# Optimization experiments

Measured on AMD Instinct MI355X. Metric: run time of the kernel, lower is better.

Reference implementation:

```python
import jax, jax.numpy as jnp
import numpy as np

LEAK = 0.95
THRESHOLD = 1.0
CLAMP = 3.0
LN_EPS = 1e-5


def setup_inputs() -> dict:
    key = jax.random.key(0)
    k1, k2 = jax.random.split(key)
    B, S, V, D = 8, 2048, 57344, 1536
    token_ids = jax.random.randint(k1, (B, S), 0, V, dtype=jnp.int64)
    emb_table = jax.random.normal(k2, (V, D), dtype=jnp.float32) * 0.02
    gamma = jnp.ones((D,), dtype=jnp.float32)
    beta = jnp.zeros((D,), dtype=jnp.float32)
    return {"token_ids": token_ids, "emb_table": emb_table, "gamma": gamma, "beta": beta}


def _layernorm(x, gamma, beta):
    mu = jnp.mean(x, axis=-1, keepdims=True)
    var = jnp.mean(jnp.square(x - mu), axis=-1, keepdims=True)
    return (x - mu) * jax.lax.rsqrt(var + LN_EPS) * gamma + beta


def _lif_scan(x):
    # x: [B, S, D]; sequential LIF recurrence over time axis S
    B, S, D = x.shape
    v0 = jnp.zeros((B, D), dtype=x.dtype)

    def step(v, xt):
        v = v * LEAK + xt
        v = jnp.clip(v, -CLAMP, CLAMP)
        spike = (v >= THRESHOLD).astype(x.dtype)
        return v * (1.0 - spike), spike

    _, spikes = jax.lax.scan(step, v0, jnp.swapaxes(x, 0, 1))  # spikes: [S, B, D]
    return jnp.swapaxes(spikes, 0, 1)


def reference(token_ids, emb_table, gamma, beta):
    x = emb_table[token_ids]          # [B, S, D] embedding lookup
    x = _layernorm(x, gamma, beta)    # continuous residual stream
    spikes = _lif_scan(x)             # 0/1 spike tensor [B, S, D]
    return spikes, x
```

## Files before the change

### kernel.cpp

```cpp
#include <hip/hip_runtime.h>


constexpr int Bv = 8, Sv = 2048, Dv = 1536;
constexpr int Cn = 32;
constexpr int Ln = Sv / Cn;
constexpr int Wn = 64;
constexpr int BD = Bv * Dv;
constexpr int TNMAX = Ln + Wn;

constexpr size_t FLAG_OFF  = 0;
constexpr size_t STATS_OFF = 64;
constexpr size_t SPEC0_OFF = STATS_OFF + (size_t)2 * Bv * Sv * 8;
constexpr size_t SPEC1_OFF = SPEC0_OFF + (size_t)Cn * BD * 8;
constexpr size_t WS_NEED   = SPEC1_OFF + (size_t)Cn * BD * 8;

__device__ __forceinline__ double ln_x64(float e, double mu, double rs,
                                         double gd, double bd) {
#pragma clang fp contract(off)
    return (((double)e - mu) * rs) * gd + bd;
}
__device__ __forceinline__ double lif_step(double v, double x, bool& spike) {
#pragma clang fp contract(off)
    double vv = v * 0.95;
    vv = vv + x;
    vv = fmin(fmax(vv, -3.0), 3.0);
    spike = (vv >= 1.0);
    return spike ? 0.0 : vv;
}

extern "C" __global__ __launch_bounds__(256)
void detect_tok64(const int* __restrict__ tok, int* __restrict__ flag)
{
    __shared__ int any_nz;
    if (threadIdx.x == 0) any_nz = 0;
    __syncthreads();
    int nz = 0;
    for (int i = threadIdx.x; i < (Bv * Sv) / 2; i += 256) nz |= tok[2 * i + 1];
    if (nz) atomicOr(&any_nz, 1);
    __syncthreads();
    if (threadIdx.x == 0) flag[0] = (any_nz == 0) ? 1 : 0;
}

extern "C" __global__ __launch_bounds__(128)
void ln_stats_kernel(const int* __restrict__ tok,
                     const float* __restrict__ emb,
                     const float* __restrict__ gamma,
                     const float* __restrict__ beta,
                     float* __restrict__ x_out,
                     double* __restrict__ stats,
                     const int* __restrict__ tok64_flag)
{
#pragma clang fp contract(off)
    __shared__ double p1[2], p2[2];

    const int row = blockIdx.x;
    const int t   = threadIdx.x;
    const int lane = t & 63, wave = t >> 6;

    const int shift = tok64_flag[0];
    const long long tk = (long long)tok[(size_t)row << shift];
    const float* src = emb + tk * (long long)Dv;

    float4 xv[3];
#pragma unroll
    for (int k = 0; k < 3; ++k) xv[k] = reinterpret_cast<const float4*>(src)[t + 128 * k];

    double s = 0.0;
#pragma unroll
    for (int k = 0; k < 3; ++k) {
        s += (double)xv[k].x; s += (double)xv[k].y;
        s += (double)xv[k].z; s += (double)xv[k].w;
    }
#pragma unroll
    for (int off = 1; off < 64; off <<= 1) s += __shfl_xor(s, off);
    if (lane == 0) p1[wave] = s;
    __syncthreads();
    const double mu = (p1[0] + p1[1]) / 1536.0;

    double q = 0.0;
#pragma unroll
    for (int k = 0; k < 3; ++k) {
        double d0 = (double)xv[k].x - mu; q += d0 * d0;
        double d1 = (double)xv[k].y - mu; q += d1 * d1;
        double d2 = (double)xv[k].z - mu; q += d2 * d2;
        double d3 = (double)xv[k].w - mu; q += d3 * d3;
    }
#pragma unroll
    for (int off = 1; off < 64; off <<= 1) q += __shfl_xor(q, off);
    if (lane == 0) p2[wave] = q;
    __syncthreads();
    const double var  = (p2[0] + p2[1]) / 1536.0;
    const double rstd = 1.0 / sqrt(var + 1e-5);

    if (t == 0) { stats[2 * row] = mu; stats[2 * row + 1] = rstd; }

    float* dst = x_out + (long long)row * Dv;
#pragma unroll
    for (int k = 0; k < 3; ++k) {
        const int f4 = t + 128 * k;
        const float4 g4 = reinterpret_cast<const float4*>(gamma)[f4];
        const float4 b4 = reinterpret_cast<const float4*>(beta)[f4];
        float4 o;
        o.x = (float)((((double)xv[k].x - mu) * rstd) * (double)g4.x + (double)b4.x);
        o.y = (float)((((double)xv[k].y - mu) * rstd) * (double)g4.y + (double)b4.y);
        o.z = (float)((((double)xv[k].z - mu) * rstd) * (double)g4.z + (double)b4.z);
        o.w = (float)((((double)xv[k].w - mu) * rstd) * (double)g4.w + (double)b4.w);
        reinterpret_cast<float4*>(dst)[f4] = o;
    }
}

extern "C" __global__ __launch_bounds__(256)
void lif64_spec(const int* __restrict__ tok,
                const float* __restrict__ emb,
                const float* __restrict__ gamma,
                const float* __restrict__ beta,
                const double* __restrict__ stats,
                float* __restrict__ spk,
                double* __restrict__ spec_start,
                double* __restrict__ spec_end,
                const int* __restrict__ tok64_flag)
{
    constexpr int DBLK = Dv / 256;
    __shared__ int     tokl[TNMAX];
    __shared__ double2 statl[TNMAX];

    const int t    = threadIdx.x;
    const int bid  = blockIdx.x;
    const int dblk = bid % DBLK;
    const int c    = (bid / DBLK) % Cn;
    const int b    = bid / (DBLK * Cn);
    const int d    = dblk * 256 + t;

    const int s0 = c * Ln;
    const int sw = (c == 0) ? 0 : s0 - Wn;
    const int TN = s0 + Ln - sw;
    const int warm = s0 - sw;
    const int rowbase = b * Sv;

    if (t < TN) {
        const int row = rowbase + sw + t;
        const int shift = tok64_flag[0];
        tokl[t]  = tok[(size_t)row << shift];
        statl[t] = reinterpret_cast<const double2*>(stats)[row];
    }
    __syncthreads();

    const double gd = (double)gamma[d];
    const double bd = (double)beta[d];
    float* sp = spk + (size_t)b * Sv * Dv + d;

    constexpr int U = 8;
    float ecur[U], enxt[U];
#pragma unroll
    for (int k = 0; k < U; ++k)
        ecur[k] = emb[(long long)tokl[k] * Dv + d];

    double v = 0.0, vstart = 0.0;
    for (int i = 0; i < TN; i += U) {
        if (i + U < TN) {
#pragma unroll
            for (int k = 0; k < U; ++k)
                enxt[k] = emb[(long long)tokl[i + U + k] * Dv + d];
        }
#pragma unroll
        for (int k = 0; k < U; ++k) {
            const int idx = i + k;
            if (idx == warm) vstart = v;
            const double2 st = statl[idx];
            const double x = ln_x64(ecur[k], st.x, st.y, gd, bd);
            bool spike;
            const double vn = lif_step(v, x, spike);
            if (idx >= warm)
                __builtin_nontemporal_store(spike ? 1.0f : 0.0f,
                                            &sp[(size_t)(sw + idx) * Dv]);
            v = vn;
        }
#pragma unroll
        for (int k = 0; k < U; ++k) ecur[k] = enxt[k];
    }

    const size_t chain = (size_t)b * Dv + d;
    spec_start[(size_t)c * BD + chain] = vstart;
    spec_end[(size_t)c * BD + chain]   = v;
}

extern "C" __global__ __launch_bounds__(64)
void lif64_fixup(const int* __restrict__ tok,
                 const float* __restrict__ emb,
                 const float* __restrict__ gamma,
                 const float* __restrict__ beta,
                 const double* __restrict__ stats,
                 const double* __restrict__ spec_start,
                 const double* __restrict__ spec_end,
                 float* __restrict__ spk,
                 const int* __restrict__ tok64_flag)
{
    const int gid = blockIdx.x * 64 + threadIdx.x;
    const int b = gid / Dv;
    const int d = gid - b * Dv;
    const int shift = tok64_flag[0];
    const double gd = (double)gamma[d];
    const double bd = (double)beta[d];
    const int rowbase = b * Sv;
    float* sp = spk + (size_t)b * Sv * Dv + d;

    double v = 0.0;
    for (int c = 0; c < Cn; ++c) {
        const double vs = spec_start[(size_t)c * BD + gid];
        const double ve = spec_end[(size_t)c * BD + gid];
        if (v == vs) { v = ve; continue; }
        constexpr int U = 8;
        const int s0 = c * Ln;
        float  ecur[U], enxt[U];
        double mcur[U], mnxt[U], rcur[U], rnxt[U];
#pragma unroll
        for (int k = 0; k < U; ++k) {
            const int row = rowbase + s0 + k;
            const long long tk = (long long)tok[(size_t)row << shift];
            ecur[k] = emb[tk * (long long)Dv + d];
            mcur[k] = stats[2 * row];
            rcur[k] = stats[2 * row + 1];
        }
        for (int i = 0; i < Ln; i += U) {
            if (i + U < Ln) {
#pragma unroll
                for (int k = 0; k < U; ++k) {
                    const int row = rowbase + s0 + i + U + k;
                    const long long tk = (long long)tok[(size_t)row << shift];
                    enxt[k] = emb[tk * (long long)Dv + d];
                    mnxt[k] = stats[2 * row];
                    rnxt[k] = stats[2 * row + 1];
                }
            }
#pragma unroll
            for (int k = 0; k < U; ++k) {
                const double x = ln_x64(ecur[k], mcur[k], rcur[k], gd, bd);
                bool spike;
                v = lif_step(v, x, spike);
                sp[(size_t)(s0 + i + k) * Dv] = spike ? 1.0f : 0.0f;
            }
#pragma unroll
            for (int k = 0; k < U; ++k) {
                ecur[k] = enxt[k]; mcur[k] = mnxt[k]; rcur[k] = rnxt[k];
            }
        }
    }
}

extern "C" __global__ __launch_bounds__(64)
void lif64_seq(const int* __restrict__ tok,
               const float* __restrict__ emb,
               const float* __restrict__ gamma,
               const float* __restrict__ beta,
               const double* __restrict__ stats,
               float* __restrict__ spk,
               const int* __restrict__ tok64_flag)
{
    const int gid = blockIdx.x * 64 + threadIdx.x;
    const int b = gid / Dv;
    const int d = gid - b * Dv;
    const int shift = tok64_flag[0];
    const int rowbase = b * Sv;
    const double gd = (double)gamma[d];
    const double bd = (double)beta[d];
    float* sp = spk + (size_t)b * Sv * Dv + d;

    constexpr int U = 8;
    float  ecur[U], enxt[U];
    double mcur[U], mnxt[U], rcur[U], rnxt[U];
#pragma unroll
    for (int k = 0; k < U; ++k) {
        const int row = rowbase + k;
        const long long tk = (long long)tok[(size_t)row << shift];
        ecur[k] = emb[tk * (long long)Dv + d];
        mcur[k] = stats[2 * row];
        rcur[k] = stats[2 * row + 1];
    }
    double v = 0.0;
    for (int s = 0; s < Sv; s += U) {
        if (s + U < Sv) {
#pragma unroll
            for (int k = 0; k < U; ++k) {
                const int row = rowbase + s + U + k;
                const long long tk = (long long)tok[(size_t)row << shift];
                enxt[k] = emb[tk * (long long)Dv + d];
                mnxt[k] = stats[2 * row];
                rnxt[k] = stats[2 * row + 1];
            }
        }
#pragma unroll
        for (int k = 0; k < U; ++k) {
            const double x = ln_x64(ecur[k], mcur[k], rcur[k], gd, bd);
            bool spike;
            v = lif_step(v, x, spike);
            __builtin_nontemporal_store(spike ? 1.0f : 0.0f, &sp[(size_t)(s + k) * Dv]);
        }
#pragma unroll
        for (int k = 0; k < U; ++k) { ecur[k] = enxt[k]; mcur[k] = mnxt[k]; rcur[k] = rnxt[k]; }
    }
}

extern "C" void kernel_launch(void* const* d_in, const int* in_sizes, int n_in,
                              void* d_out, int out_size, void* d_ws, size_t ws_size,
                              hipStream_t stream)
{
    const int*   tok   = (const int*)  d_in[0];
    const float* emb   = (const float*)d_in[1];
    const float* gamma = (const float*)d_in[2];
    const float* beta  = (const float*)d_in[3];

    float* out = (float*)d_out;
    float* spk = out;
    float* x   = out + (size_t)Bv * Sv * Dv;

    int*    flg   = (int*)((char*)d_ws + FLAG_OFF);
    double* stats = (double*)((char*)d_ws + STATS_OFF);

    detect_tok64<<<1, 256, 0, stream>>>(tok, flg);
    ln_stats_kernel<<<Bv * Sv, 128, 0, stream>>>(tok, emb, gamma, beta, x, stats, flg);

    if (ws_size >= WS_NEED) {
        double* spec0 = (double*)((char*)d_ws + SPEC0_OFF);
        double* spec1 = (double*)((char*)d_ws + SPEC1_OFF);
        lif64_spec<<<Bv * Cn * (Dv / 256), 256, 0, stream>>>(
            tok, emb, gamma, beta, stats, spk, spec0, spec1, flg);
        lif64_fixup<<<BD / 64, 64, 0, stream>>>(
            tok, emb, gamma, beta, stats, spec0, spec1, spk, flg);
    } else {
        lif64_seq<<<BD / 64, 64, 0, stream>>>(tok, emb, gamma, beta, stats, spk, flg);
    }
}
```

Measured before the change: 118.9 us.

## Pack LIF spikes into 64-bit masks and expand in a separate kernel

The speculative and fixup LIF kernels now record each chunk's spikes as a 64-bit mask in workspace instead of writing float spikes directly. A new spike_expand kernel then writes the full float spike tensor once, using nontemporal stores. This keeps the fixup pass from rewriting spike rows it has to recompute, and takes the large strided store traffic off the sequential scan. In exchange it adds a kernel launch and extra workspace. The token-width detection kernel also moves from 256 to 1024 threads.

```diff
diff --git a/kernel.cpp b/kernel.cpp
--- a/kernel.cpp
+++ b/kernel.cpp
@@ -12,7 +12,8 @@
 constexpr size_t STATS_OFF = 64;
 constexpr size_t SPEC0_OFF = STATS_OFF + (size_t)2 * Bv * Sv * 8;
 constexpr size_t SPEC1_OFF = SPEC0_OFF + (size_t)Cn * BD * 8;
-constexpr size_t WS_NEED   = SPEC1_OFF + (size_t)Cn * BD * 8;
+constexpr size_t BITS_OFF  = SPEC1_OFF + (size_t)Cn * BD * 8;
+constexpr size_t WS_NEED   = BITS_OFF + (size_t)Cn * BD * 8;
 
 __device__ __forceinline__ double ln_x64(float e, double mu, double rs,
                                          double gd, double bd) {
@@ -28,14 +29,14 @@
     return spike ? 0.0 : vv;
 }
 
-extern "C" __global__ __launch_bounds__(256)
+extern "C" __global__ __launch_bounds__(1024)
 void detect_tok64(const int* __restrict__ tok, int* __restrict__ flag)
 {
     __shared__ int any_nz;
     if (threadIdx.x == 0) any_nz = 0;
     __syncthreads();
     int nz = 0;
-    for (int i = threadIdx.x; i < (Bv * Sv) / 2; i += 256) nz |= tok[2 * i + 1];
+    for (int i = threadIdx.x; i < (Bv * Sv) / 2; i += 1024) nz |= tok[2 * i + 1];
     if (nz) atomicOr(&any_nz, 1);
     __syncthreads();
     if (threadIdx.x == 0) flag[0] = (any_nz == 0) ? 1 : 0;
@@ -115,9 +116,9 @@
                 const float* __restrict__ gamma,
                 const float* __restrict__ beta,
                 const double* __restrict__ stats,
-                float* __restrict__ spk,
                 double* __restrict__ spec_start,
                 double* __restrict__ spec_end,
+                unsigned long long* __restrict__ bits,
                 const int* __restrict__ tok64_flag)
 {
     constexpr int DBLK = Dv / 256;
@@ -147,7 +148,6 @@
 
     const double gd = (double)gamma[d];
     const double bd = (double)beta[d];
-    float* sp = spk + (size_t)b * Sv * Dv + d;
 
     constexpr int U = 8;
     float ecur[U], enxt[U];
@@ -156,6 +156,7 @@
         ecur[k] = emb[(long long)tokl[k] * Dv + d];
 
     double v = 0.0, vstart = 0.0;
+    unsigned long long m = 0;
     for (int i = 0; i < TN; i += U) {
         if (i + U < TN) {
 #pragma unroll
@@ -169,11 +170,9 @@
             const double2 st = statl[idx];
             const double x = ln_x64(ecur[k], st.x, st.y, gd, bd);
             bool spike;
-            const double vn = lif_step(v, x, spike);
+            v = lif_step(v, x, spike);
             if (idx >= warm)
-                __builtin_nontemporal_store(spike ? 1.0f : 0.0f,
-                                            &sp[(size_t)(sw + idx) * Dv]);
-            v = vn;
+                m |= (unsigned long long)spike << (idx - warm);
         }
 #pragma unroll
         for (int k = 0; k < U; ++k) ecur[k] = enxt[k];
@@ -182,6 +181,7 @@
     const size_t chain = (size_t)b * Dv + d;
     spec_start[(size_t)c * BD + chain] = vstart;
     spec_end[(size_t)c * BD + chain]   = v;
+    bits[(size_t)c * BD + chain]       = m;
 }
 
 extern "C" __global__ __launch_bounds__(64)
@@ -192,7 +192,7 @@
                  const double* __restrict__ stats,
                  const double* __restrict__ spec_start,
                  const double* __restrict__ spec_end,
-                 float* __restrict__ spk,
+                 unsigned long long* __restrict__ bits,
                  const int* __restrict__ tok64_flag)
 {
     const int gid = blockIdx.x * 64 + threadIdx.x;
@@ -202,7 +202,6 @@
     const double gd = (double)gamma[d];
     const double bd = (double)beta[d];
     const int rowbase = b * Sv;
-    float* sp = spk + (size_t)b * Sv * Dv + d;
 
     double v = 0.0;
     for (int c = 0; c < Cn; ++c) {
@@ -221,6 +220,7 @@
             mcur[k] = stats[2 * row];
             rcur[k] = stats[2 * row + 1];
         }
+        unsigned long long m = 0;
         for (int i = 0; i < Ln; i += U) {
             if (i + U < Ln) {
 #pragma unroll
@@ -237,14 +237,35 @@
                 const double x = ln_x64(ecur[k], mcur[k], rcur[k], gd, bd);
                 bool spike;
                 v = lif_step(v, x, spike);
-                sp[(size_t)(s0 + i + k) * Dv] = spike ? 1.0f : 0.0f;
+                m |= (unsigned long long)spike << (i + k);
             }
 #pragma unroll
             for (int k = 0; k < U; ++k) {
                 ecur[k] = enxt[k]; mcur[k] = mnxt[k]; rcur[k] = rnxt[k];
             }
         }
-    }
+        bits[(size_t)c * BD + gid] = m;
+    }
+}
+
+extern "C" __global__ __launch_bounds__(256)
+void spike_expand(const unsigned long long* __restrict__ bits,
+                  float* __restrict__ spk)
+{
+    constexpr int DBLK = Dv / 256;
+    const int t    = threadIdx.x;
+    const int bid  = blockIdx.x;
+    const int dblk = bid % DBLK;
+    const int c    = (bid / DBLK) % Cn;
+    const int b    = bid / (DBLK * Cn);
+    const int d    = dblk * 256 + t;
+
+    const unsigned long long m = bits[(size_t)c * BD + (size_t)b * Dv + d];
+    float* sp = spk + ((size_t)b * Sv + (size_t)c * Ln) * Dv + d;
+#pragma unroll
+    for (int s = 0; s < Ln; ++s)
+        __builtin_nontemporal_store(((m >> s) & 1ull) ? 1.0f : 0.0f,
+                                    &sp[(size_t)s * Dv]);
 }
 
 extern "C" __global__ __launch_bounds__(64)
@@ -316,16 +337,18 @@
     int*    flg   = (int*)((char*)d_ws + FLAG_OFF);
     double* stats = (double*)((char*)d_ws + STATS_OFF);
 
-    detect_tok64<<<1, 256, 0, stream>>>(tok, flg);
+    detect_tok64<<<1, 1024, 0, stream>>>(tok, flg);
     ln_stats_kernel<<<Bv * Sv, 128, 0, stream>>>(tok, emb, gamma, beta, x, stats, flg);
 
     if (ws_size >= WS_NEED) {
         double* spec0 = (double*)((char*)d_ws + SPEC0_OFF);
         double* spec1 = (double*)((char*)d_ws + SPEC1_OFF);
+        unsigned long long* bits = (unsigned long long*)((char*)d_ws + BITS_OFF);
         lif64_spec<<<Bv * Cn * (Dv / 256), 256, 0, stream>>>(
-            tok, emb, gamma, beta, stats, spk, spec0, spec1, flg);
+            tok, emb, gamma, beta, stats, spec0, spec1, bits, flg);
         lif64_fixup<<<BD / 64, 64, 0, stream>>>(
-            tok, emb, gamma, beta, stats, spec0, spec1, spk, flg);
+            tok, emb, gamma, beta, stats, spec0, spec1, bits, flg);
+        spike_expand<<<Bv * Cn * (Dv / 256), 256, 0, stream>>>(bits, spk);
     } else {
         lif64_seq<<<BD / 64, 64, 0, stream>>>(tok, emb, gamma, beta, stats, spk, flg);
     }
```

After: 151.2 us. +27.1%, slower.
